# Performance work log

Measured on AMD Instinct MI355X. Metric: run time of the kernel, lower is better.

Reference implementation:

```python
import jax, jax.numpy as jnp
import numpy as np

B, T, S = 32, 64, 128
ENC_H, DEC_H, ATTN, EMB = 512, 512, 256, 256
VOCAB, PAD = 32000, 0


def setup_inputs() -> dict:
    key = jax.random.key(0)
    ks = jax.random.split(key, 12)
    emb = jax.random.normal(ks[0], (VOCAB, EMB), jnp.float32) * 0.02
    emb = emb.at[PAD].set(0.0)  # padding_idx row zeroed
    in_dim = EMB + ENC_H
    return {
        "y_decoder_input": jax.random.randint(ks[1], (B, T), 0, VOCAB, jnp.int32),
        "encoder_outputs": jax.random.normal(ks[2], (B, S, ENC_H), jnp.float32),
        "decoder_init": jax.random.normal(ks[3], (1, B, DEC_H), jnp.float32),
        "encoder_mask": jnp.ones((B, S), jnp.int32),
        "embedding": emb,
        "W_enc": jax.random.normal(ks[4], (ENC_H, ATTN), jnp.float32) * 0.02,
        "W_dec": jax.random.normal(ks[5], (DEC_H, ATTN), jnp.float32) * 0.02,
        "v": jax.random.normal(ks[6], (ATTN,), jnp.float32) * 0.02,
        "W_ih": jax.random.normal(ks[7], (3 * DEC_H, in_dim), jnp.float32) * 0.02,
        "W_hh": jax.random.normal(ks[8], (3 * DEC_H, DEC_H), jnp.float32) * 0.02,
        "b_ih": jnp.zeros((3 * DEC_H,), jnp.float32),
        "b_hh": jnp.zeros((3 * DEC_H,), jnp.float32),
        "W_fc": jax.random.normal(ks[9], (DEC_H, VOCAB - 1), jnp.float32) * 0.02,
        "b_fc": jnp.zeros((VOCAB - 1,), jnp.float32),
    }


def reference(y_decoder_input, encoder_outputs, decoder_init, encoder_mask,
              embedding, W_enc, W_dec, v, W_ih, W_hh, b_ih, b_hh, W_fc, b_fc):
    H = decoder_init.shape[-1]
    embedded = embedding[y_decoder_input]            # [B,T,E]
    enc_proj = encoder_outputs @ W_enc               # [B,S,A] hoisted out of loop
    mask0 = encoder_mask == 0                        # [B,S]

    def step(h, emb_t):
        prev = h[-1]                                 # [B,H]
        # additive attention
        dec = prev @ W_dec                           # [B,A]
        energy = jnp.tanh(enc_proj + dec[:, None, :]) @ v   # [B,S]
        energy = jnp.where(mask0, -1e9, energy)
        aw = jax.nn.softmax(energy, axis=1)          # [B,S]
        context = jnp.einsum('bs,bsd->bd', aw, encoder_outputs)
        x = jnp.concatenate([emb_t, context], axis=1)  # [B, E+ENC_H]
        # GRU cell (PyTorch gate order r, z, n)
        gx = x @ W_ih.T + b_ih                       # [B,3H]
        gh = prev @ W_hh.T + b_hh                    # [B,3H]
        xr, xz, xn = gx[:, :H], gx[:, H:2*H], gx[:, 2*H:]
        hr, hz, hn = gh[:, :H], gh[:, H:2*H], gh[:, 2*H:]
        r = jax.nn.sigmoid(xr + hr)
        z = jax.nn.sigmoid(xz + hz)
        n = jnp.tanh(xn + r * hn)
        h_new = (1.0 - z) * n + z * prev
        out = h_new @ W_fc + b_fc                    # [B,V-1]
        return h_new[None], (out, aw)

    _, (outs, aws) = jax.lax.scan(step, decoder_init, jnp.swapaxes(embedded, 0, 1))
    outputs = jnp.swapaxes(outs, 0, 1)               # [B,T,V-1]
    attn_weights = jnp.swapaxes(aws, 0, 1)           # [B,T,S]
    return outputs, attn_weights
```

## Files before the change

kernel.cpp:

```cpp
#include <hip/hip_runtime.h>
#include <hip/hip_bf16.h>
#include <hip/hip_cooperative_groups.h>
#include <cstdint>
#include <cstddef>

namespace cg = cooperative_groups;

#define B_   32
#define T_   64
#define S_   128
#define EH   512
#define DH   512
#define ATT  256
#define EMBD 256
#define V_   32000
#define VO   31999
#define G3   1536

#define ATTN_OFF 65533952

typedef __attribute__((ext_vector_type(8))) short bf16x8;
typedef __attribute__((ext_vector_type(4))) float f32x4;

static __device__ __forceinline__ unsigned short f2bf(float f) {
    union { float f; unsigned u; } x; x.f = f;
    unsigned r = (x.u + 0x7fffu + ((x.u >> 16) & 1u)) >> 16;
    return (unsigned short)r;
}

static __device__ __forceinline__ float fast_tanh(float x) {
    float xc = fminf(fmaxf(x, -15.0f), 15.0f);
    float e = __expf(2.0f * xc);
    return (e - 1.0f) / (e + 1.0f);
}

static __device__ __forceinline__ float fast_sig(float x) {
    return 1.0f / (1.0f + __expf(-x));
}

__global__ void k_trans_512x256(const float* __restrict__ in, float* __restrict__ out) {
    __shared__ float tile[32][33];
    int c0 = blockIdx.x * 32;
    int r0 = blockIdx.y * 32;
    int tx = threadIdx.x, ty = threadIdx.y;
#pragma unroll
    for (int q = 0; q < 4; q++)
        tile[ty + q*8][tx] = in[(r0 + ty + q*8) * 256 + c0 + tx];
    __syncthreads();
#pragma unroll
    for (int q = 0; q < 4; q++)
        out[(c0 + ty + q*8) * 512 + r0 + tx] = tile[tx][ty + q*8];
}

__global__ void k_wfc(const float* __restrict__ wfc, unsigned short* __restrict__ outT) {
    __shared__ float tile[32][33];
    int n0 = blockIdx.x * 32;
    int k0 = blockIdx.y * 32;
    int tx = threadIdx.x, ty = threadIdx.y;
#pragma unroll
    for (int q = 0; q < 4; q++) {
        int k = k0 + ty + q*8;
        int n = n0 + tx;
        tile[ty + q*8][tx] = (n < VO) ? wfc[(size_t)k * VO + n] : 0.0f;
    }
    __syncthreads();
#pragma unroll
    for (int q = 0; q < 4; q++) {
        int n = n0 + ty + q*8;
        int k = k0 + tx;
        outT[(size_t)n * 512 + k] = f2bf(tile[tx][ty + q*8]);
    }
}

__global__ void k_wpack(const float* __restrict__ W_ih, const float* __restrict__ W_hh,
                        unsigned short* __restrict__ Wp) {
    int idx = blockIdx.x * 256 + threadIdx.x;
    int e    = idx & 7;
    int lane = (idx >> 3) & 63;
    int q    = (idx >> 9) & 3;
    int kc   = (idx >> 11) & 31;
    int j    = idx >> 16;
    int io = lane & 15, ko = lane >> 4;
    int i = j * 16 + io;
    int k = kc * 32 + ko * 8 + e;
    int n = (q == 0) ? i : (q == 1) ? (512 + i) : (1024 + i);
    float val;
    if (k < 512) {
        val = (q == 3) ? 0.0f : W_ih[(size_t)n * 768 + 256 + k];
    } else {
        val = (q == 2) ? 0.0f : W_hh[(size_t)n * 512 + (k - 512)];
    }
    Wp[idx] = f2bf(val);
}

__global__ void k_hinit2(const float* __restrict__ di, float* __restrict__ h32,
                         unsigned short* __restrict__ Xf0) {
    int idx = blockIdx.x * 256 + threadIdx.x;
    float val = di[idx];
    h32[idx] = val;
    int b = idx >> 9, i = idx & 511;
    int mt = b >> 4, io = b & 15;
    int kc = 16 + (i >> 5), ko = (i >> 3) & 3, e = i & 7;
    Xf0[((((mt * 32 + kc) * 64) + ko * 16 + io) << 3) + e] = f2bf(val);
}

__global__ __launch_bounds__(256) void k_encproj(const float* __restrict__ enc,
                                                 const float* __restrict__ WencT,
                                                 float* __restrict__ ep) {
    int row0 = blockIdx.x * 16;
    int n = threadIdx.x;
    const float* wr = WencT + (size_t)n * 512;
    float acc[16];
#pragma unroll
    for (int r = 0; r < 16; r++) acc[r] = 0.0f;
    for (int k = 0; k < 512; k += 4) {
        float4 w = *(const float4*)(wr + k);
#pragma unroll
        for (int r = 0; r < 16; r++) {
            float4 x = *(const float4*)(enc + (size_t)(row0 + r) * 512 + k);
            acc[r] += x.x * w.x + x.y * w.y + x.z * w.z + x.w * w.w;
        }
    }
#pragma unroll
    for (int r = 0; r < 16; r++)
        ep[(size_t)(row0 + r) * 256 + n] = acc[r];
}

__global__ __launch_bounds__(256) void k_gxemb(const int* __restrict__ y,
                                               const float* __restrict__ embt,
                                               const float* __restrict__ W_ih,
                                               const float* __restrict__ bih,
                                               float* __restrict__ gx) {
    int row0 = blockIdx.y * 16;
    int col = blockIdx.x * 256 + threadIdx.x;
    const float* wr = W_ih + (size_t)col * 768;
    float acc[16];
#pragma unroll
    for (int r = 0; r < 16; r++) acc[r] = 0.0f;
    for (int k = 0; k < 256; k += 4) {
        float4 w = *(const float4*)(wr + k);
#pragma unroll
        for (int r = 0; r < 16; r++) {
            const float* xr = embt + (size_t)y[row0 + r] * 256 + k;
            float4 x = *(const float4*)xr;
            acc[r] += x.x * w.x + x.y * w.y + x.z * w.z + x.w * w.w;
        }
    }
    float bv = bih[col];
#pragma unroll
    for (int r = 0; r < 16; r++)
        gx[(size_t)(row0 + r) * G3 + col] = acc[r] + bv;
}

__global__ __launch_bounds__(512) void k_recur(
        const float* __restrict__ WdecT, const float* __restrict__ ep,
        const float* __restrict__ v, const int* __restrict__ mask,
        const float* __restrict__ enc, float* __restrict__ attn_out,
        const unsigned short* __restrict__ Wp, const float* __restrict__ gx_emb,
        const float* __restrict__ b_hh, const float* __restrict__ dinit,
        unsigned short* __restrict__ Xf0, unsigned short* __restrict__ Xf1,
        float* __restrict__ h32, unsigned short* __restrict__ Hall) {
    __shared__ uint4 Wlds4[6144];
    __shared__ float hbuf[512];
    __shared__ float decp[512];
    __shared__ float es[128];
    __shared__ float red[2];
    __shared__ float vs[256];
    __shared__ int   msk[128];
    __shared__ float bhs[48];
    __shared__ float hloc[512];
    __shared__ float pacc[2048];

    cg::grid_group grid = cg::this_grid();

    int bid = blockIdx.x, tid = threadIdx.x;
    int b = bid;
    int j = bid;
    int w = tid >> 6, lane = tid & 63;

    char* WldsB = (char*)Wlds4;

    for (int it = 0; it < 12; it++) {
        int cid = it * 512 + tid;
        int c = cid >> 6, off = cid & 63;
        int q, kc;
        if (c < 32)      { q = 0; kc = c; }
        else if (c < 64) { q = 1; kc = c - 32; }
        else if (c < 80) { q = 2; kc = c - 64; }
        else             { q = 3; kc = c - 80 + 16; }
        const uint4* src = (const uint4*)Wp + ((size_t)((j * 32 + kc) * 4 + q) << 6) + off;
        Wlds4[c * 64 + off] = *src;
    }
    if (tid < 256) vs[tid] = v[tid];
    if (tid < 128) msk[tid] = mask[b * 128 + tid];
    if (tid < 48)  bhs[tid] = b_hh[(tid >> 4) * 512 + j * 16 + (tid & 15)];
    hloc[tid] = dinit[(size_t)(tid >> 4) * 512 + j * 16 + (tid & 15)];
    __syncthreads();

    const float* epb  = ep  + (size_t)b * 128 * 256;
    const float* encb = enc + (size_t)b * 128 * 512;

    for (int t = 0; t < T_; t++) {
        unsigned short* Xcur = (t & 1) ? Xf1 : Xf0;
        unsigned short* Xnxt = (t & 1) ? Xf0 : Xf1;

        hbuf[tid] = h32[b * 512 + tid];
        __syncthreads();
        {
            int d = tid & 255, half = tid >> 8;
            const float* wr = WdecT + (size_t)d * 512 + half * 256;
            const float* hb = hbuf + half * 256;
            float acc = 0.0f;
#pragma unroll 8
            for (int k = 0; k < 256; k += 4) {
                float4 wv = *(const float4*)(wr + k);
                float4 xv = *(const float4*)(hb + k);
                acc += xv.x * wv.x + xv.y * wv.y + xv.z * wv.z + xv.w * wv.w;
            }
            decp[tid] = acc;
        }
        __syncthreads();
        if (tid < 256) decp[tid] += decp[tid + 256];
        __syncthreads();
        {
            float d0 = decp[lane], d1 = decp[lane + 64],
                  d2 = decp[lane + 128], d3 = decp[lane + 192];
            float v0 = vs[lane], v1 = vs[lane + 64],
                  v2 = vs[lane + 128], v3 = vs[lane + 192];
#pragma unroll
            for (int si = 0; si < 16; si++) {
                int s = w * 16 + si;
                const float* er = epb + (size_t)s * 256;
                float e = fast_tanh(er[lane] + d0) * v0
                        + fast_tanh(er[lane + 64] + d1) * v1
                        + fast_tanh(er[lane + 128] + d2) * v2
                        + fast_tanh(er[lane + 192] + d3) * v3;
#pragma unroll
                for (int o = 32; o; o >>= 1) e += __shfl_xor(e, o);
                if (lane == 0)
                    es[s] = (msk[s] == 0) ? -1e9f : e;
            }
        }
        __syncthreads();
        if (tid < 64) {
            float a = fmaxf(es[tid], es[tid + 64]);
#pragma unroll
            for (int o = 32; o; o >>= 1) a = fmaxf(a, __shfl_xor(a, o));
            if (tid == 0) red[0] = a;
        }
        __syncthreads();
        float mx = red[0];
        if (tid < 128) es[tid] = __expf(es[tid] - mx);
        __syncthreads();
        if (tid < 64) {
            float a = es[tid] + es[tid + 64];
#pragma unroll
            for (int o = 32; o; o >>= 1) a += __shfl_xor(a, o);
            if (tid == 0) red[1] = a;
        }
        __syncthreads();
        float inv = 1.0f / red[1];
        if (tid < 128) {
            float aw = es[tid] * inv;
            es[tid] = aw;
            attn_out[(size_t)b * (T_ * S_) + t * S_ + tid] = aw;
        }
        __syncthreads();
        {
            float a1 = 0.0f;
            const float* eb = encb + tid;
#pragma unroll 8
            for (int s = 0; s < 128; s++)
                a1 += es[s] * eb[(size_t)s * 512];
            int d = tid;
            int hw = (((b >> 4) * 32 + (d >> 5)) * 64 + ((d >> 3) & 3) * 16 + (b & 15)) * 8 + (d & 7);
            Xcur[hw] = f2bf(a1);
        }
        grid.sync();

        float ge_r, ge_z, ge_n;
        int gb = tid >> 4, gi = j * 16 + (tid & 15);
        {
            const float* g = gx_emb + (size_t)(gb * 64 + t) * G3;
            ge_r = g[gi]; ge_z = g[512 + gi]; ge_n = g[1024 + gi];
        }
        if (w < 6) {
            int mt = w & 1, g = w >> 1;
            const uint4* Xg = (const uint4*)Xcur;
            f32x4 acc0 = {0.f, 0.f, 0.f, 0.f};
            f32x4 acc1 = {0.f, 0.f, 0.f, 0.f};
            if (g < 2) {
                const char* wb = WldsB + (g ? 32768 : 0);
#pragma unroll
                for (int kc = 0; kc < 32; kc++) {
                    uint4 av = Xg[(mt * 32 + kc) * 64 + lane];
                    bf16x8 bv = *(const bf16x8*)(wb + kc * 1024 + lane * 16);
                    acc0 = __builtin_amdgcn_mfma_f32_16x16x32_bf16(*(const bf16x8*)&av, bv, acc0, 0, 0, 0);
                }
            } else {
#pragma unroll
                for (int kc = 0; kc < 16; kc++) {
                    uint4 av = Xg[(mt * 32 + kc) * 64 + lane];
                    bf16x8 bv = *(const bf16x8*)(WldsB + 65536 + kc * 1024 + lane * 16);
                    acc0 = __builtin_amdgcn_mfma_f32_16x16x32_bf16(*(const bf16x8*)&av, bv, acc0, 0, 0, 0);
                }
#pragma unroll
                for (int kc = 16; kc < 32; kc++) {
                    uint4 av = Xg[(mt * 32 + kc) * 64 + lane];
                    bf16x8 bv = *(const bf16x8*)(WldsB + 81920 + (kc - 16) * 1024 + lane * 16);
                    acc1 = __builtin_amdgcn_mfma_f32_16x16x32_bf16(*(const bf16x8*)&av, bv, acc1, 0, 0, 0);
                }
            }
            int row = lane >> 4, col = lane & 15;
            if (g < 2) {
#pragma unroll
                for (int reg = 0; reg < 4; reg++)
                    pacc[((g * 2 + mt) * 16 + row * 4 + reg) * 16 + col] = acc0[reg];
            } else {
#pragma unroll
                for (int reg = 0; reg < 4; reg++)
                    pacc[((2 * 2 + mt) * 16 + row * 4 + reg) * 16 + col] = acc0[reg];
#pragma unroll
                for (int reg = 0; reg < 4; reg++)
                    pacc[((3 * 2 + mt) * 16 + row * 4 + reg) * 16 + col] = acc1[reg];
            }
        }
        __syncthreads();
        {
            int i2 = tid & 15;
            int mt = gb >> 4, rrow = gb & 15;
            float rp = pacc[((0 * 2 + mt) * 16 + rrow) * 16 + i2];
            float zp = pacc[((1 * 2 + mt) * 16 + rrow) * 16 + i2];
            float nx = pacc[((2 * 2 + mt) * 16 + rrow) * 16 + i2];
            float nh = pacc[((3 * 2 + mt) * 16 + rrow) * 16 + i2];
            float r = fast_sig(ge_r + rp + bhs[i2]);
            float z = fast_sig(ge_z + zp + bhs[16 + i2]);
            float n = fast_tanh(ge_n + nx + r * (nh + bhs[32 + i2]));
            float prev = hloc[tid];
            float hv = (1.0f - z) * n + z * prev;
            hloc[tid] = hv;
            h32[gb * 512 + gi] = hv;
            unsigned short hb16 = f2bf(hv);
            int i = gi;
            int hw = ((mt * 32 + 16 + (i >> 5)) * 64 + ((i >> 3) & 3) * 16 + rrow) * 8 + (i & 7);
            Xnxt[hw] = hb16;
            Hall[(size_t)(gb * 64 + t) * 512 + i] = hb16;
        }
        grid.sync();
    }
}

__global__ __launch_bounds__(256) void k_fc(const unsigned short* __restrict__ A,
                                            const unsigned short* __restrict__ Bt,
                                            const float* __restrict__ bias,
                                            float* __restrict__ out) {
    __shared__ char smem[65536];
    unsigned short* Abuf = (unsigned short*)smem;
    unsigned short* Bbuf = (unsigned short*)(smem + 10240);
    int tid = threadIdx.x;
    int n0 = blockIdx.x * 128, m0 = blockIdx.y * 128;
    int w = tid >> 6, lane = tid & 63;
    int wm = w >> 1, wn = w & 1;
    int io = lane & 15, ko = lane >> 4;

    const uint4* Ag = (const uint4*)A;
    const uint4* Bg = (const uint4*)Bt;

    f32x4 z4 = {0.f, 0.f, 0.f, 0.f};
    f32x4 acc[4][4];
#pragma unroll
    for (int a = 0; a < 4; a++)
#pragma unroll
        for (int b = 0; b < 4; b++) acc[a][b] = z4;

    for (int k0 = 0; k0 < 512; k0 += 32) {
        uint4 av[2], bv[2];
#pragma unroll
        for (int u = 0; u < 2; u++) {
            int c = tid + u * 256;
            int r = c >> 2, ch = c & 3;
            av[u] = Ag[(size_t)(m0 + r) * 64 + (k0 >> 3) + ch];
            bv[u] = Bg[(size_t)(n0 + r) * 64 + (k0 >> 3) + ch];
        }
        __syncthreads();
#pragma unroll
        for (int u = 0; u < 2; u++) {
            int c = tid + u * 256;
            int r = c >> 2, ch = c & 3;
            *(uint4*)((char*)Abuf + r * 80 + ch * 16) = av[u];
            *(uint4*)((char*)Bbuf + r * 80 + ch * 16) = bv[u];
        }
        __syncthreads();
        bf16x8 af[4], bf[4];
#pragma unroll
        for (int s = 0; s < 4; s++) {
            af[s] = *(const bf16x8*)((char*)Abuf + (wm * 64 + s * 16 + io) * 80 + ko * 16);
            bf[s] = *(const bf16x8*)((char*)Bbuf + (wn * 64 + s * 16 + io) * 80 + ko * 16);
        }
#pragma unroll
        for (int sm = 0; sm < 4; sm++)
#pragma unroll
            for (int sn = 0; sn < 4; sn++)
                acc[sm][sn] = __builtin_amdgcn_mfma_f32_16x16x32_bf16(af[sm], bf[sn], acc[sm][sn], 0, 0, 0);
    }

    __syncthreads();
    float* Cst = (float*)smem;
#pragma unroll
    for (int sm = 0; sm < 4; sm++)
#pragma unroll
        for (int sn = 0; sn < 4; sn++) {
            int cc = wn * 64 + sn * 16 + io;
#pragma unroll
            for (int reg = 0; reg < 4; reg++) {
                int rr = wm * 64 + sm * 16 + ko * 4 + reg;
                Cst[rr * 128 + cc] = acc[sm][sn][reg];
            }
        }
    __syncthreads();
    {
        int c = tid & 127, rh = tid >> 7;
        int ng = n0 + c;
        if (ng < VO) {
            float bv = bias[ng];
#pragma unroll 8
            for (int i = 0; i < 64; i++) {
                int r = i * 2 + rh;
                out[(size_t)(m0 + r) * VO + ng] = Cst[r * 128 + c] + bv;
            }
        }
    }
}

extern "C" void kernel_launch(void* const* d_in, const int* in_sizes, int n_in,
                              void* d_out, int out_size, void* d_ws, size_t ws_size,
                              hipStream_t stream) {
    const int*   y      = (const int*)d_in[0];
    const float* enc    = (const float*)d_in[1];
    const float* dinit  = (const float*)d_in[2];
    const int*   mask   = (const int*)d_in[3];
    const float* embt   = (const float*)d_in[4];
    const float* W_enc  = (const float*)d_in[5];
    const float* W_dec  = (const float*)d_in[6];
    const float* v      = (const float*)d_in[7];
    const float* W_ih   = (const float*)d_in[8];
    const float* W_hh   = (const float*)d_in[9];
    const float* b_ih   = (const float*)d_in[10];
    const float* b_hh   = (const float*)d_in[11];
    const float* W_fc   = (const float*)d_in[12];
    const float* b_fc   = (const float*)d_in[13];
    float* out = (float*)d_out;

    char* ws = (char*)d_ws;
    size_t o = 0;
    float* enc_proj = (float*)(ws + o);          o += (size_t)4096 * 256 * 4;
    float* gx_emb   = (float*)(ws + o);          o += (size_t)2048 * 1536 * 4;
    float* WencT    = (float*)(ws + o);          o += (size_t)256 * 512 * 4;
    float* WdecT    = (float*)(ws + o);          o += (size_t)256 * 512 * 4;
    unsigned short* Wp   = (unsigned short*)(ws + o); o += (size_t)2097152 * 2;
    unsigned short* WfcT = (unsigned short*)(ws + o); o += (size_t)32000 * 512 * 2;
    unsigned short* Hall = (unsigned short*)(ws + o); o += (size_t)2048 * 512 * 2;
    unsigned short* Xf0  = (unsigned short*)(ws + o); o += (size_t)32768 * 2;
    unsigned short* Xf1  = (unsigned short*)(ws + o); o += (size_t)32768 * 2;
    float* h32 = (float*)(ws + o);               o += (size_t)32 * 512 * 4;

    k_trans_512x256<<<dim3(8, 16), dim3(32, 8), 0, stream>>>(W_enc, WencT);
    k_trans_512x256<<<dim3(8, 16), dim3(32, 8), 0, stream>>>(W_dec, WdecT);
    k_wfc<<<dim3(1000, 16), dim3(32, 8), 0, stream>>>(W_fc, WfcT);
    k_wpack<<<8192, 256, 0, stream>>>(W_ih, W_hh, Wp);
    k_hinit2<<<64, 256, 0, stream>>>(dinit, h32, Xf0);
    k_encproj<<<256, 256, 0, stream>>>(enc, WencT, enc_proj);
    k_gxemb<<<dim3(6, 128), 256, 0, stream>>>(y, embt, W_ih, b_ih, gx_emb);

    float* attn_out = out + ATTN_OFF;

    {
        const float* WdecT_c = WdecT; const float* ep_c = enc_proj;
        const unsigned short* Wp_c = Wp; const float* gx_c = gx_emb;
        void* args[] = {
            (void*)&WdecT_c, (void*)&ep_c, (void*)&v, (void*)&mask,
            (void*)&enc, (void*)&attn_out, (void*)&Wp_c, (void*)&gx_c,
            (void*)&b_hh, (void*)&dinit, (void*)&Xf0, (void*)&Xf1,
            (void*)&h32, (void*)&Hall
        };
        hipLaunchCooperativeKernel((void*)k_recur, dim3(32), dim3(512),
                                   args, 0, stream);
    }

    k_fc<<<dim3(250, 16), 256, 0, stream>>>(Hall, WfcT, b_fc, out);
}
```

Measured before the change: 3.094 ms.

## Replace cooperative grid.sync with custom atomic barrier and relaxed agent-scope accesses

```diff
diff --git a/kernel.cpp b/kernel.cpp
--- a/kernel.cpp
+++ b/kernel.cpp
@@ -3,8 +3,6 @@
 #include <hip/hip_cooperative_groups.h>
 #include <cstdint>
 #include <cstddef>
-
-namespace cg = cooperative_groups;
 
 #define B_   32
 #define T_   64
@@ -36,6 +34,30 @@
 
 static __device__ __forceinline__ float fast_sig(float x) {
     return 1.0f / (1.0f + __expf(-x));
+}
+
+static __device__ __forceinline__ bf16x8 ldfrag(const unsigned long long* p) {
+    union { unsigned long long u[2]; bf16x8 v; } x;
+    x.u[0] = __hip_atomic_load(p,     __ATOMIC_RELAXED, __HIP_MEMORY_SCOPE_AGENT);
+    x.u[1] = __hip_atomic_load(p + 1, __ATOMIC_RELAXED, __HIP_MEMORY_SCOPE_AGENT);
+    return x.v;
+}
+
+static __device__ __forceinline__ void gbar(unsigned* cnt, unsigned* gen,
+                                            unsigned target) {
+    __syncthreads();
+    if (threadIdx.x == 0) {
+        unsigned old = __hip_atomic_fetch_add(cnt, 1u, __ATOMIC_RELEASE,
+                                              __HIP_MEMORY_SCOPE_AGENT);
+        if (old == 31u) {
+            __hip_atomic_store(cnt, 0u, __ATOMIC_RELAXED, __HIP_MEMORY_SCOPE_AGENT);
+            __hip_atomic_store(gen, target, __ATOMIC_RELEASE, __HIP_MEMORY_SCOPE_AGENT);
+        } else {
+            while (__hip_atomic_load(gen, __ATOMIC_RELAXED,
+                                     __HIP_MEMORY_SCOPE_AGENT) != target) {}
+        }
+    }
+    __syncthreads();
 }
 
 __global__ void k_trans_512x256(const float* __restrict__ in, float* __restrict__ out) {
@@ -94,7 +116,7 @@
 }
 
 __global__ void k_hinit2(const float* __restrict__ di, float* __restrict__ h32,
-                         unsigned short* __restrict__ Xf0) {
+                         unsigned short* __restrict__ Xf0, unsigned* __restrict__ bar) {
     int idx = blockIdx.x * 256 + threadIdx.x;
     float val = di[idx];
     h32[idx] = val;
@@ -102,6 +124,7 @@
     int mt = b >> 4, io = b & 15;
     int kc = 16 + (i >> 5), ko = (i >> 3) & 3, e = i & 7;
     Xf0[((((mt * 32 + kc) * 64) + ko * 16 + io) << 3) + e] = f2bf(val);
+    if (idx == 0) { bar[0] = 0u; bar[1] = 0u; }
 }
 
 __global__ __launch_bounds__(256) void k_encproj(const float* __restrict__ enc,
@@ -159,7 +182,8 @@
         const unsigned short* __restrict__ Wp, const float* __restrict__ gx_emb,
         const float* __restrict__ b_hh, const float* __restrict__ dinit,
         unsigned short* __restrict__ Xf0, unsigned short* __restrict__ Xf1,
-        float* __restrict__ h32, unsigned short* __restrict__ Hall) {
+        float* __restrict__ h32, unsigned short* __restrict__ Hall,
+        unsigned* __restrict__ bar) {
     __shared__ uint4 Wlds4[6144];
     __shared__ float hbuf[512];
     __shared__ float decp[512];
@@ -170,8 +194,7 @@
     __shared__ float bhs[48];
     __shared__ float hloc[512];
     __shared__ float pacc[2048];
-
-    cg::grid_group grid = cg::this_grid();
+    __shared__ unsigned g0s;
 
     int bid = blockIdx.x, tid = threadIdx.x;
     int b = bid;
@@ -179,6 +202,8 @@
     int w = tid >> 6, lane = tid & 63;
 
     char* WldsB = (char*)Wlds4;
+    unsigned* bcnt = bar;
+    unsigned* bgen = bar + 1;
 
     for (int it = 0; it < 12; it++) {
         int cid = it * 512 + tid;
@@ -195,7 +220,10 @@
     if (tid < 128) msk[tid] = mask[b * 128 + tid];
     if (tid < 48)  bhs[tid] = b_hh[(tid >> 4) * 512 + j * 16 + (tid & 15)];
     hloc[tid] = dinit[(size_t)(tid >> 4) * 512 + j * 16 + (tid & 15)];
-    __syncthreads();
+    if (tid == 0)
+        g0s = __hip_atomic_load(bgen, __ATOMIC_RELAXED, __HIP_MEMORY_SCOPE_AGENT);
+    __syncthreads();
+    unsigned bt = g0s;
 
     const float* epb  = ep  + (size_t)b * 128 * 256;
     const float* encb = enc + (size_t)b * 128 * 512;
@@ -204,7 +232,8 @@
         unsigned short* Xcur = (t & 1) ? Xf1 : Xf0;
         unsigned short* Xnxt = (t & 1) ? Xf0 : Xf1;
 
-        hbuf[tid] = h32[b * 512 + tid];
+        hbuf[tid] = __hip_atomic_load(&h32[b * 512 + tid], __ATOMIC_RELAXED,
+                                      __HIP_MEMORY_SCOPE_AGENT);
         __syncthreads();
         {
             int d = tid & 255, half = tid >> 8;
@@ -273,10 +302,16 @@
             for (int s = 0; s < 128; s++)
                 a1 += es[s] * eb[(size_t)s * 512];
             int d = tid;
+            unsigned short mybf = f2bf(a1);
+            int oth = __shfl_down((int)mybf, 1);
             int hw = (((b >> 4) * 32 + (d >> 5)) * 64 + ((d >> 3) & 3) * 16 + (b & 15)) * 8 + (d & 7);
-            Xcur[hw] = f2bf(a1);
-        }
-        grid.sync();
+            if (!(d & 1)) {
+                unsigned pk = ((unsigned)mybf & 0xffffu) | ((unsigned)oth << 16);
+                __hip_atomic_store((unsigned*)Xcur + (hw >> 1), pk,
+                                   __ATOMIC_RELAXED, __HIP_MEMORY_SCOPE_AGENT);
+            }
+        }
+        gbar(bcnt, bgen, ++bt);
 
         float ge_r, ge_z, ge_n;
         int gb = tid >> 4, gi = j * 16 + (tid & 15);
@@ -286,29 +321,29 @@
         }
         if (w < 6) {
             int mt = w & 1, g = w >> 1;
-            const uint4* Xg = (const uint4*)Xcur;
+            const unsigned long long* Xg8 = (const unsigned long long*)Xcur;
             f32x4 acc0 = {0.f, 0.f, 0.f, 0.f};
             f32x4 acc1 = {0.f, 0.f, 0.f, 0.f};
             if (g < 2) {
                 const char* wb = WldsB + (g ? 32768 : 0);
 #pragma unroll
                 for (int kc = 0; kc < 32; kc++) {
-                    uint4 av = Xg[(mt * 32 + kc) * 64 + lane];
+                    bf16x8 av = ldfrag(Xg8 + (size_t)((mt * 32 + kc) * 64 + lane) * 2);
                     bf16x8 bv = *(const bf16x8*)(wb + kc * 1024 + lane * 16);
-                    acc0 = __builtin_amdgcn_mfma_f32_16x16x32_bf16(*(const bf16x8*)&av, bv, acc0, 0, 0, 0);
+                    acc0 = __builtin_amdgcn_mfma_f32_16x16x32_bf16(av, bv, acc0, 0, 0, 0);
                 }
             } else {
 #pragma unroll
                 for (int kc = 0; kc < 16; kc++) {
-                    uint4 av = Xg[(mt * 32 + kc) * 64 + lane];
+                    bf16x8 av = ldfrag(Xg8 + (size_t)((mt * 32 + kc) * 64 + lane) * 2);
                     bf16x8 bv = *(const bf16x8*)(WldsB + 65536 + kc * 1024 + lane * 16);
-                    acc0 = __builtin_amdgcn_mfma_f32_16x16x32_bf16(*(const bf16x8*)&av, bv, acc0, 0, 0, 0);
+                    acc0 = __builtin_amdgcn_mfma_f32_16x16x32_bf16(av, bv, acc0, 0, 0, 0);
                 }
 #pragma unroll
                 for (int kc = 16; kc < 32; kc++) {
-                    uint4 av = Xg[(mt * 32 + kc) * 64 + lane];
+                    bf16x8 av = ldfrag(Xg8 + (size_t)((mt * 32 + kc) * 64 + lane) * 2);
                     bf16x8 bv = *(const bf16x8*)(WldsB + 81920 + (kc - 16) * 1024 + lane * 16);
-                    acc1 = __builtin_amdgcn_mfma_f32_16x16x32_bf16(*(const bf16x8*)&av, bv, acc1, 0, 0, 0);
+                    acc1 = __builtin_amdgcn_mfma_f32_16x16x32_bf16(av, bv, acc1, 0, 0, 0);
                 }
             }
             int row = lane >> 4, col = lane & 15;
@@ -339,14 +374,20 @@
             float prev = hloc[tid];
             float hv = (1.0f - z) * n + z * prev;
             hloc[tid] = hv;
-            h32[gb * 512 + gi] = hv;
+            __hip_atomic_store(&h32[gb * 512 + gi], hv, __ATOMIC_RELAXED,
+                               __HIP_MEMORY_SCOPE_AGENT);
             unsigned short hb16 = f2bf(hv);
+            int oth = __shfl_down((int)hb16, 1);
             int i = gi;
             int hw = ((mt * 32 + 16 + (i >> 5)) * 64 + ((i >> 3) & 3) * 16 + rrow) * 8 + (i & 7);
-            Xnxt[hw] = hb16;
+            if (!(tid & 1)) {
+                unsigned pk = ((unsigned)hb16 & 0xffffu) | ((unsigned)oth << 16);
+                __hip_atomic_store((unsigned*)Xnxt + (hw >> 1), pk,
+                                   __ATOMIC_RELAXED, __HIP_MEMORY_SCOPE_AGENT);
+            }
             Hall[(size_t)(gb * 64 + t) * 512 + i] = hb16;
         }
-        grid.sync();
+        gbar(bcnt, bgen, ++bt);
     }
 }
 
@@ -463,12 +504,13 @@
     unsigned short* Xf0  = (unsigned short*)(ws + o); o += (size_t)32768 * 2;
     unsigned short* Xf1  = (unsigned short*)(ws + o); o += (size_t)32768 * 2;
     float* h32 = (float*)(ws + o);               o += (size_t)32 * 512 * 4;
+    unsigned* bar = (unsigned*)(ws + o);         o += 256;
 
     k_trans_512x256<<<dim3(8, 16), dim3(32, 8), 0, stream>>>(W_enc, WencT);
     k_trans_512x256<<<dim3(8, 16), dim3(32, 8), 0, stream>>>(W_dec, WdecT);
     k_wfc<<<dim3(1000, 16), dim3(32, 8), 0, stream>>>(W_fc, WfcT);
     k_wpack<<<8192, 256, 0, stream>>>(W_ih, W_hh, Wp);
-    k_hinit2<<<64, 256, 0, stream>>>(dinit, h32, Xf0);
+    k_hinit2<<<64, 256, 0, stream>>>(dinit, h32, Xf0, bar);
     k_encproj<<<256, 256, 0, stream>>>(enc, WencT, enc_proj);
     k_gxemb<<<dim3(6, 128), 256, 0, stream>>>(y, embt, W_ih, b_ih, gx_emb);
 
@@ -481,7 +523,7 @@
             (void*)&WdecT_c, (void*)&ep_c, (void*)&v, (void*)&mask,
             (void*)&enc, (void*)&attn_out, (void*)&Wp_c, (void*)&gx_c,
             (void*)&b_hh, (void*)&dinit, (void*)&Xf0, (void*)&Xf1,
-            (void*)&h32, (void*)&Hall
+            (void*)&h32, (void*)&Hall, (void*)&bar
         };
         hipLaunchCooperativeKernel((void*)k_recur, dim3(32), dim3(512),
                                    args, 0, stream);
```

Measured after the change: 3.073 ms. Within noise of the previous version (-0.7%).
